# Kernel optimization log

Hardware: AMD Instinct MI355X
Metric: run time of the kernel (lower is better)

## Reference

```python
import jax, jax.numpy as jnp
import numpy as np

WINDOWS = (5, 5, 25, 25)  # per-layer neighborhood window sizes
N_HEAD = 4


def _na2d(x, wqkv, bqkv, wo, bo, window, n_head):
    """2D neighborhood (NATTEN-style) attention, channels-last x: [B,H,W,C].
    Each query attends to a window x window neighborhood whose start is
    clamped so the window stays inside the image (NATTEN boundary rule)."""
    B, H, W, C = x.shape
    hd = C // n_head
    qkv = x @ wqkv + bqkv                      # [B,H,W,3C]
    q, k, v = jnp.split(qkv, 3, axis=-1)
    q = q.reshape(B, H, W, n_head, hd) * (hd ** -0.5)
    k = k.reshape(B, H, W, n_head, hd)
    v = v.reshape(B, H, W, n_head, hd)
    half = window // 2
    sh = jnp.clip(jnp.arange(H) - half, 0, H - window)   # window start per row
    sw = jnp.clip(jnp.arange(W) - half, 0, W - window)
    ih = sh[:, None] + jnp.arange(window)                # [H, window]
    iw = sw[:, None] + jnp.arange(window)                # [W, window]
    # gather K/V neighborhoods -> [B,H,W,window,window,n_head,hd]
    kn = k[:, ih[:, None, :, None], iw[None, :, None, :]]
    vn = v[:, ih[:, None, :, None], iw[None, :, None, :]]
    scores = jnp.einsum('bhwnd,bhwijnd->bhwnij', q, kn)
    kk = window * window
    att = jax.nn.softmax(scores.reshape(B, H, W, n_head, kk), axis=-1)
    out = jnp.einsum('bhwnk,bhwknd->bhwnd', att,
                     vn.reshape(B, H, W, kk, n_head, hd))
    return out.reshape(B, H, W, C) @ wo + bo


def setup_inputs() -> dict:
    key = jax.random.key(0)
    ks = jax.random.split(key, 5)
    B, T, F, C = 1, 64, 352, 24   # batch, time frames, CQT bins (88*4), n_unit
    L = len(WINDOWS)
    s = 1.0 / np.sqrt(C)
    return {
        'x': jax.random.normal(ks[0], (B, T, F, C), jnp.float32),
        'qkv_w': jax.random.normal(ks[1], (L, C, 3 * C), jnp.float32) * s,
        'qkv_b': jax.random.normal(ks[2], (L, 3 * C), jnp.float32) * 0.01,
        'out_w': jax.random.normal(ks[3], (L, C, C), jnp.float32) * s,
        'out_b': jax.random.normal(ks[4], (L, C), jnp.float32) * 0.01,
    }


def reference(x, qkv_w, qkv_b, out_w, out_b):
    for i, win in enumerate(WINDOWS):
        res = x
        x = _na2d(x, qkv_w[i], qkv_b[i], out_w[i], out_b[i], win, N_HEAD) + res
        if i < 2:
            # F.max_pool2d(kernel=(2,1)) on (B,H,W,C) layout pools the W dim by 2
            B, H, W, C = x.shape
            x = x.reshape(B, H, W // 2, 2, C).max(axis=3)
    return jnp.swapaxes(x, -2, -1)   # x.transpose(-2, -1)
```

## Files before the change

kernel.cpp:

```cpp
#include <hip/hip_runtime.h>
#include <cstdint>

#define QSCALE 0.40824829046386301636f

__global__ __launch_bounds__(256) void qkv_first(
    const float* __restrict__ x, const float* __restrict__ w,
    const float* __restrict__ b, float* __restrict__ q,
    float* __restrict__ kv, int npx)
{
  __shared__ __align__(16) float swT[72 * 24];
  __shared__ float sb[72];
  for (int i = threadIdx.x; i < 1728; i += 256) swT[(i % 72) * 24 + i / 72] = w[i];
  if (threadIdx.x < 72) sb[threadIdx.x] = b[threadIdx.x];
  __syncthreads();
  const int t = blockIdx.x * 256 + threadIdx.x;
  const int p = t >> 2, jg = t & 3;
  if (p >= npx) return;
  float xr[24];
  const float4* xp = (const float4*)(x + (size_t)p * 24);
#pragma unroll
  for (int i = 0; i < 6; ++i) {
    const float4 f = xp[i];
    xr[4*i] = f.x; xr[4*i+1] = f.y; xr[4*i+2] = f.z; xr[4*i+3] = f.w;
  }
#pragma unroll
  for (int jj = 0; jj < 18; ++jj) {
    const int j = jg * 18 + jj;
    const float* wr = &swT[j * 24];
    float acc = sb[j];
#pragma unroll
    for (int c = 0; c < 24; ++c) acc += xr[c] * wr[c];
    if (j < 24)      q[((size_t)(j / 6) * npx + p) * 6 + j % 6] = acc * QSCALE;
    else if (j < 48) { const int u = j - 24; kv[((size_t)(u / 6) * npx + p) * 12 + u % 6] = acc; }
    else             { const int u = j - 48; kv[((size_t)(u / 6) * npx + p) * 12 + 6 + u % 6] = acc; }
  }
}

__global__ __launch_bounds__(128) void attn5(
    const float* __restrict__ q, const float* __restrict__ kv,
    float* __restrict__ att, int H, int W)
{
  __shared__ __align__(16) float skv[12 * 12 * 12];
  const int tid = threadIdx.x;
  const int h0 = blockIdx.y * 8, w0 = blockIdx.x * 8, hd = blockIdx.z;
  const int N = H * W;
  const int rlo = min(max(h0 - 2, 0), H - 5);
  const int nr  = min(max(h0 + 5, 0), H - 5) + 4 - rlo + 1;
  const int clo = min(max(w0 - 2, 0), W - 5);
  const int nc  = min(max(w0 + 5, 0), W - 5) + 4 - clo + 1;
  const float* kvh = kv + (size_t)hd * N * 12;
  const int ncc = nc * 3;
  for (int i = tid; i < nr * ncc; i += 128) {
    const int r = i / ncc, c4 = i - r * ncc;
    const float4 v = ((const float4*)(kvh + ((size_t)(rlo + r) * W + clo) * 12))[c4];
    ((float4*)skv)[r * 36 + c4] = v;
  }
  __syncthreads();

  const int ql = tid >> 1, sr = tid & 1;
  const int qh = h0 + (ql >> 3), qw = w0 + (ql & 7);
  const float* qp = q + ((size_t)hd * N + (size_t)qh * W + qw) * 6;
  const float q0 = qp[0], q1 = qp[1], q2 = qp[2], q3 = qp[3], q4 = qp[4], q5 = qp[5];
  const int shq = min(max(qh - 2, 0), H - 5) - rlo;
  const int swq = min(max(qw - 2, 0), W - 5) - clo;

  float m = -1e30f, l = 0.f, a0 = 0, a1 = 0, a2 = 0, a3 = 0, a4 = 0, a5 = 0;
  for (int rr = sr; rr < 5; rr += 2) {
    const float* rowp = skv + ((shq + rr) * 12 + swq) * 12;
#pragma unroll
    for (int cc = 0; cc < 5; ++cc) {
      const float* p = rowp + cc * 12;
      const float4 A = *(const float4*)p;
      const float4 B = *(const float4*)(p + 4);
      const float4 C = *(const float4*)(p + 8);
      const float s = q0*A.x + q1*A.y + q2*A.z + q3*A.w + q4*B.x + q5*B.y;
      float d = s - m;
      if (d > 8.0f) {
        const float r2 = __expf(-d);
        l *= r2; a0 *= r2; a1 *= r2; a2 *= r2; a3 *= r2; a4 *= r2; a5 *= r2;
        m = s; d = 0.f;
      }
      const float e = __expf(d);
      l += e;
      a0 += e*B.z; a1 += e*B.w; a2 += e*C.x;
      a3 += e*C.y; a4 += e*C.z; a5 += e*C.w;
    }
  }
  {
    const float om = __shfl_xor(m, 1), ol = __shfl_xor(l, 1);
    const float o0 = __shfl_xor(a0, 1), o1 = __shfl_xor(a1, 1), o2 = __shfl_xor(a2, 1);
    const float o3 = __shfl_xor(a3, 1), o4 = __shfl_xor(a4, 1), o5 = __shfl_xor(a5, 1);
    const float nm = fmaxf(m, om);
    const float f1 = __expf(m - nm), f2 = __expf(om - nm);
    l = l*f1 + ol*f2;
    a0 = a0*f1 + o0*f2; a1 = a1*f1 + o1*f2; a2 = a2*f1 + o2*f2;
    a3 = a3*f1 + o3*f2; a4 = a4*f1 + o4*f2; a5 = a5*f1 + o5*f2;
  }
  if (sr == 0) {
    const float inv = 1.0f / l;
    float* ap = att + ((size_t)qh * W + qw) * 24 + hd * 6;
    ((float2*)ap)[0] = make_float2(a0*inv, a1*inv);
    ((float2*)ap)[1] = make_float2(a2*inv, a3*inv);
    ((float2*)ap)[2] = make_float2(a4*inv, a5*inv);
  }
}

__global__ __launch_bounds__(256) void attn25(
    const float* __restrict__ q, const float* __restrict__ kv,
    float* __restrict__ att)
{
  constexpr int H = 64, W = 88, N = H * W;
  constexpr int RS = 388;
  __shared__ __align__(16) float skv[28 * RS];
  const int tid = threadIdx.x;
  const int h0 = blockIdx.y * 4, w0 = blockIdx.x * 8, hd = blockIdx.z;
  const int rlo = min(max(h0 - 12, 0), H - 25);
  const int nr  = min(max(h0 + 3 - 12, 0), H - 25) + 24 - rlo + 1;
  const int clo = min(max(w0 - 12, 0), W - 25);
  const int nc  = min(max(w0 + 7 - 12, 0), W - 25) + 24 - clo + 1;
  const float* kvh = kv + (size_t)hd * N * 12;
  const int ncc = nc * 3;
  for (int i = tid; i < nr * ncc; i += 256) {
    const int r = i / ncc, c4 = i - r * ncc;
    const float4 v = ((const float4*)(kvh + ((size_t)(rlo + r) * W + clo) * 12))[c4];
    ((float4*)skv)[r * (RS / 4) + c4] = v;
  }
  __syncthreads();

  const int qw_ = tid >> 5, slice = tid & 31, sr = slice >> 2, sc = slice & 3;
  const int qw = w0 + qw_;
  const int swq = min(max(qw - 12, 0), W - 25) - clo;

  float qv[4][6];
  int srel[4];
#pragma unroll
  for (int qi = 0; qi < 4; ++qi) {
    const float* qp = q + ((size_t)hd * N + (size_t)(h0 + qi) * W + qw) * 6;
#pragma unroll
    for (int d = 0; d < 6; ++d) qv[qi][d] = qp[d];
    srel[qi] = min(max(h0 + qi - 12, 0), H - 25) - rlo;
  }

  float m_[4], l_[4], acc[4][6];
#pragma unroll
  for (int qi = 0; qi < 4; ++qi) {
    m_[qi] = -1e30f; l_[qi] = 0.f;
#pragma unroll
    for (int d = 0; d < 6; ++d) acc[qi][d] = 0.f;
  }

  for (int rg = sr; rg < nr; rg += 8) {
    const float* rowp = skv + rg * RS + swq * 12;
    for (int cc = sc; cc < 25; cc += 4) {
      const float* p = rowp + cc * 12;
      const float4 A = *(const float4*)p;
      const float4 B = *(const float4*)(p + 4);
      const float4 C = *(const float4*)(p + 8);
#pragma unroll
      for (int qi = 0; qi < 4; ++qi) {
        if (rg >= srel[qi] && rg <= srel[qi] + 24) {
          const float s = qv[qi][0]*A.x + qv[qi][1]*A.y + qv[qi][2]*A.z
                        + qv[qi][3]*A.w + qv[qi][4]*B.x + qv[qi][5]*B.y;
          float d = s - m_[qi];
          if (d > 8.0f) {
            const float r2 = __expf(-d);
            l_[qi] *= r2;
            acc[qi][0] *= r2; acc[qi][1] *= r2; acc[qi][2] *= r2;
            acc[qi][3] *= r2; acc[qi][4] *= r2; acc[qi][5] *= r2;
            m_[qi] = s; d = 0.f;
          }
          const float e = __expf(d);
          l_[qi] += e;
          acc[qi][0] += e*B.z; acc[qi][1] += e*B.w; acc[qi][2] += e*C.x;
          acc[qi][3] += e*C.y; acc[qi][4] += e*C.z; acc[qi][5] += e*C.w;
        }
      }
    }
  }

#pragma unroll
  for (int mask = 1; mask <= 16; mask <<= 1) {
#pragma unroll
    for (int qi = 0; qi < 4; ++qi) {
      const float om = __shfl_xor(m_[qi], mask), ol = __shfl_xor(l_[qi], mask);
      float oa[6];
#pragma unroll
      for (int d = 0; d < 6; ++d) oa[d] = __shfl_xor(acc[qi][d], mask);
      const float nm = fmaxf(m_[qi], om);
      const float f1 = __expf(m_[qi] - nm), f2 = __expf(om - nm);
      m_[qi] = nm;
      l_[qi] = l_[qi]*f1 + ol*f2;
#pragma unroll
      for (int d = 0; d < 6; ++d) acc[qi][d] = acc[qi][d]*f1 + oa[d]*f2;
    }
  }
  if (slice == 0) {
#pragma unroll
    for (int qi = 0; qi < 4; ++qi) {
      const float inv = 1.0f / l_[qi];
      float* ap = att + ((size_t)(h0 + qi) * W + qw) * 24 + hd * 6;
      ((float2*)ap)[0] = make_float2(acc[qi][0]*inv, acc[qi][1]*inv);
      ((float2*)ap)[1] = make_float2(acc[qi][2]*inv, acc[qi][3]*inv);
      ((float2*)ap)[2] = make_float2(acc[qi][4]*inv, acc[qi][5]*inv);
    }
  }
}

__global__ __launch_bounds__(256) void glue_pool(
    const float* __restrict__ att, const float* __restrict__ xres,
    const float* __restrict__ wo, const float* __restrict__ bo,
    const float* __restrict__ wq, const float* __restrict__ bq,
    float* __restrict__ xn, float* __restrict__ qn, float* __restrict__ kvn,
    int Nn)
{
  __shared__ __align__(16) float swoT[24 * 24];
  __shared__ float sbo[24];
  __shared__ __align__(16) float swqT[72 * 24];
  __shared__ float sbq[72];
  __shared__ __align__(16) float sy[128 * 28];
  const int tid = threadIdx.x;
  for (int i = tid; i < 576; i += 256) swoT[(i % 24) * 24 + i / 24] = wo[i];
  for (int i = tid; i < 1728; i += 256) swqT[(i % 72) * 24 + i / 72] = wq[i];
  if (tid < 24) sbo[tid] = bo[tid];
  if (tid < 72) sbq[tid] = bq[tid];
  __syncthreads();

  {
    const int lpx = tid >> 1, half = tid & 1;
    const size_t spx = (size_t)blockIdx.x * 128 + lpx;
    float ar[24];
    const float4* ap = (const float4*)(att + spx * 24);
#pragma unroll
    for (int i = 0; i < 6; ++i) {
      const float4 f = ap[i];
      ar[4*i] = f.x; ar[4*i+1] = f.y; ar[4*i+2] = f.z; ar[4*i+3] = f.w;
    }
    float res[12];
    const float4* rp = (const float4*)(xres + spx * 24 + half * 12);
#pragma unroll
    for (int i = 0; i < 3; ++i) {
      const float4 f = rp[i];
      res[4*i] = f.x; res[4*i+1] = f.y; res[4*i+2] = f.z; res[4*i+3] = f.w;
    }
#pragma unroll
    for (int k = 0; k < 12; ++k) {
      const int c = half * 12 + k;
      const float* wr = &swoT[c * 24];
      float acc = sbo[c] + res[k];
#pragma unroll
      for (int j = 0; j < 24; ++j) acc += ar[j] * wr[j];
      sy[lpx * 28 + c] = acc;
    }
  }
  __syncthreads();
  {
    const int ppl = tid >> 2, jg = tid & 3;
    const size_t gp = (size_t)blockIdx.x * 64 + ppl;
    float xp[24];
    const float* y0 = &sy[(2 * ppl) * 28];
    const float* y1 = &sy[(2 * ppl + 1) * 28];
#pragma unroll
    for (int c = 0; c < 24; ++c) xp[c] = fmaxf(y0[c], y1[c]);
    if (jg == 0) {
      float4* xo = (float4*)(xn + gp * 24);
#pragma unroll
      for (int i = 0; i < 6; ++i)
        xo[i] = make_float4(xp[4*i], xp[4*i+1], xp[4*i+2], xp[4*i+3]);
    }
#pragma unroll
    for (int jj = 0; jj < 18; ++jj) {
      const int j = jg * 18 + jj;
      const float* wr = &swqT[j * 24];
      float acc = sbq[j];
#pragma unroll
      for (int c = 0; c < 24; ++c) acc += xp[c] * wr[c];
      if (j < 24)      qn[((size_t)(j / 6) * Nn + gp) * 6 + j % 6] = acc * QSCALE;
      else if (j < 48) { const int u = j - 24; kvn[((size_t)(u / 6) * Nn + gp) * 12 + u % 6] = acc; }
      else             { const int u = j - 48; kvn[((size_t)(u / 6) * Nn + gp) * 12 + 6 + u % 6] = acc; }
    }
  }
}

__global__ __launch_bounds__(256) void glue_nopool(
    const float* __restrict__ att, const float* __restrict__ xres,
    const float* __restrict__ wo, const float* __restrict__ bo,
    const float* __restrict__ wq, const float* __restrict__ bq,
    float* __restrict__ xn, float* __restrict__ qn, float* __restrict__ kvn,
    int Nn)
{
  __shared__ __align__(16) float swoT[24 * 24];
  __shared__ float sbo[24];
  __shared__ __align__(16) float swqT[72 * 24];
  __shared__ float sbq[72];
  __shared__ __align__(16) float sy[64 * 28];
  const int tid = threadIdx.x;
  for (int i = tid; i < 576; i += 256) swoT[(i % 24) * 24 + i / 24] = wo[i];
  for (int i = tid; i < 1728; i += 256) swqT[(i % 72) * 24 + i / 72] = wq[i];
  if (tid < 24) sbo[tid] = bo[tid];
  if (tid < 72) sbq[tid] = bq[tid];
  __syncthreads();

  {
    const int lpx = tid >> 2, qt = tid & 3;
    const size_t spx = (size_t)blockIdx.x * 64 + lpx;
    float ar[24];
    const float4* ap = (const float4*)(att + spx * 24);
#pragma unroll
    for (int i = 0; i < 6; ++i) {
      const float4 f = ap[i];
      ar[4*i] = f.x; ar[4*i+1] = f.y; ar[4*i+2] = f.z; ar[4*i+3] = f.w;
    }
#pragma unroll
    for (int k = 0; k < 6; ++k) {
      const int c = qt * 6 + k;
      const float* wr = &swoT[c * 24];
      float acc = sbo[c] + xres[spx * 24 + c];
#pragma unroll
      for (int j = 0; j < 24; ++j) acc += ar[j] * wr[j];
      sy[lpx * 28 + c] = acc;
      xn[spx * 24 + c] = acc;
    }
  }
  __syncthreads();
  {
    const int lpx = tid >> 2, jg = tid & 3;
    const size_t gp = (size_t)blockIdx.x * 64 + lpx;
    const float* yr = &sy[lpx * 28];
    float xp[24];
#pragma unroll
    for (int c = 0; c < 24; ++c) xp[c] = yr[c];
#pragma unroll
    for (int jj = 0; jj < 18; ++jj) {
      const int j = jg * 18 + jj;
      const float* wr = &swqT[j * 24];
      float acc = sbq[j];
#pragma unroll
      for (int c = 0; c < 24; ++c) acc += xp[c] * wr[c];
      if (j < 24)      qn[((size_t)(j / 6) * Nn + gp) * 6 + j % 6] = acc * QSCALE;
      else if (j < 48) { const int u = j - 24; kvn[((size_t)(u / 6) * Nn + gp) * 12 + u % 6] = acc; }
      else             { const int u = j - 48; kvn[((size_t)(u / 6) * Nn + gp) * 12 + 6 + u % 6] = acc; }
    }
  }
}

__global__ __launch_bounds__(256) void final_out(
    const float* __restrict__ att, const float* __restrict__ xres,
    const float* __restrict__ wo, const float* __restrict__ bo,
    float* __restrict__ dout)
{
  __shared__ __align__(16) float swoT[24 * 24];
  __shared__ float sbo[24];
  const int tid = threadIdx.x;
  for (int i = tid; i < 576; i += 256) swoT[(i % 24) * 24 + i / 24] = wo[i];
  if (tid < 24) sbo[tid] = bo[tid];
  __syncthreads();
  const int lpx = tid >> 1, half = tid & 1;
  const size_t spx = (size_t)blockIdx.x * 128 + lpx;
  const int gh = (int)(spx / 88), gw = (int)(spx % 88);
  float ar[24];
  const float4* ap = (const float4*)(att + spx * 24);
#pragma unroll
  for (int i = 0; i < 6; ++i) {
    const float4 f = ap[i];
    ar[4*i] = f.x; ar[4*i+1] = f.y; ar[4*i+2] = f.z; ar[4*i+3] = f.w;
  }
  float res[12];
  const float4* rp = (const float4*)(xres + spx * 24 + half * 12);
#pragma unroll
  for (int i = 0; i < 3; ++i) {
    const float4 f = rp[i];
    res[4*i] = f.x; res[4*i+1] = f.y; res[4*i+2] = f.z; res[4*i+3] = f.w;
  }
#pragma unroll
  for (int k = 0; k < 12; ++k) {
    const int c = half * 12 + k;
    const float* wr = &swoT[c * 24];
    float acc = sbo[c] + res[k];
#pragma unroll
    for (int j = 0; j < 24; ++j) acc += ar[j] * wr[j];
    dout[((size_t)gh * 24 + c) * 88 + gw] = acc;
  }
}

extern "C" void kernel_launch(void* const* d_in, const int* in_sizes, int n_in,
                              void* d_out, int out_size, void* d_ws, size_t ws_size,
                              hipStream_t stream)
{
  const float* x      = (const float*)d_in[0];
  const float* qkv_w  = (const float*)d_in[1];
  const float* qkv_b  = (const float*)d_in[2];
  const float* out_w  = (const float*)d_in[3];
  const float* out_b  = (const float*)d_in[4];
  float* out = (float*)d_out;
  float* ws = (float*)d_ws;

  const int N0 = 64 * 352, N1 = 64 * 176, N2 = 64 * 88;
  float* q   = ws;
  float* kvb = q + (size_t)N0 * 24;
  float* att = kvb + (size_t)N0 * 48;
  float* x1  = att + (size_t)N0 * 24;
  float* x2  = x1 + (size_t)N1 * 24;
  float* x3  = x2 + (size_t)N2 * 24;

  qkv_first<<<(N0 * 4) / 256, 256, 0, stream>>>(x, qkv_w, qkv_b, q, kvb, N0);

  attn5<<<dim3(44, 8, 4), 128, 0, stream>>>(q, kvb, att, 64, 352);
  glue_pool<<<176, 256, 0, stream>>>(att, x, out_w, out_b,
                                     qkv_w + 1728, qkv_b + 72, x1, q, kvb, N1);

  attn5<<<dim3(22, 8, 4), 128, 0, stream>>>(q, kvb, att, 64, 176);
  glue_pool<<<88, 256, 0, stream>>>(att, x1, out_w + 576, out_b + 24,
                                    qkv_w + 2 * 1728, qkv_b + 2 * 72, x2, q, kvb, N2);

  attn25<<<dim3(11, 16, 4), 256, 0, stream>>>(q, kvb, att);
  glue_nopool<<<88, 256, 0, stream>>>(att, x2, out_w + 2 * 576, out_b + 2 * 24,
                                      qkv_w + 3 * 1728, qkv_b + 3 * 72, x3, q, kvb, N2);

  attn25<<<dim3(11, 16, 4), 256, 0, stream>>>(q, kvb, att);
  final_out<<<44, 256, 0, stream>>>(att, x3, out_w + 3 * 576, out_b + 3 * 24, out);
}
```

Before: 176.1 us.

## Fuse 5x5 attention with out-proj, pooling and next QKV; drop online-softmax max tracking

Merges the 5x5 neighborhood attention kernel with the following glue kernel (output projection, residual, max-pool, next-layer QKV), processing all four heads per block. The attention output no longer round-trips through global memory, and two launches per layer go away. Q/KV buffers are now double-buffered so one fused kernel can read one set while writing the next. The online-softmax running max and rescale are removed in both attention kernels in favour of plain exp sums with float2 packed FMAs, which risks overflow if scores grow large.

```diff
diff --git a/kernel.cpp b/kernel.cpp
--- a/kernel.cpp
+++ b/kernel.cpp
@@ -2,6 +2,13 @@
 #include <cstdint>
 
 #define QSCALE 0.40824829046386301636f
+
+__device__ __forceinline__ float2 pk_fma(float2 a, float2 b, float2 c) {
+  return make_float2(fmaf(a.x, b.x, c.x), fmaf(a.y, b.y, c.y));
+}
+__device__ __forceinline__ float2 pk_mul(float2 a, float2 b) {
+  return make_float2(a.x * b.x, a.y * b.y);
+}
 
 __global__ __launch_bounds__(256) void qkv_first(
     const float* __restrict__ x, const float* __restrict__ w,
@@ -36,72 +43,135 @@
   }
 }
 
-__global__ __launch_bounds__(128) void attn5(
-    const float* __restrict__ q, const float* __restrict__ kv,
-    float* __restrict__ att, int H, int W)
-{
-  __shared__ __align__(16) float skv[12 * 12 * 12];
+__global__ __launch_bounds__(256) void attn5_fused(
+    const float* __restrict__ q, const float* __restrict__ kvb,
+    const float* __restrict__ xres,
+    const float* __restrict__ wo, const float* __restrict__ bo,
+    const float* __restrict__ wq, const float* __restrict__ bq,
+    float* __restrict__ xn, float* __restrict__ qn, float* __restrict__ kvn,
+    int H, int W, int Nn)
+{
+  __shared__ __align__(16) float skv[4 * 1732];
+  __shared__ __align__(16) float satt[64 * 28];
+  __shared__ __align__(16) float swoT[24 * 24];
+  __shared__ float sbo[24];
+  __shared__ __align__(16) float swqT[72 * 24];
+  __shared__ float sbq[72];
+
   const int tid = threadIdx.x;
-  const int h0 = blockIdx.y * 8, w0 = blockIdx.x * 8, hd = blockIdx.z;
+  const int h0 = blockIdx.y * 8, w0 = blockIdx.x * 8;
   const int N = H * W;
+
+  for (int i = tid; i < 576; i += 256) swoT[(i % 24) * 24 + i / 24] = wo[i];
+  for (int i = tid; i < 1728; i += 256) swqT[(i % 72) * 24 + i / 72] = wq[i];
+  if (tid < 24) sbo[tid] = bo[tid];
+  if (tid < 72) sbq[tid] = bq[tid];
+
   const int rlo = min(max(h0 - 2, 0), H - 5);
   const int nr  = min(max(h0 + 5, 0), H - 5) + 4 - rlo + 1;
   const int clo = min(max(w0 - 2, 0), W - 5);
   const int nc  = min(max(w0 + 5, 0), W - 5) + 4 - clo + 1;
-  const float* kvh = kv + (size_t)hd * N * 12;
   const int ncc = nc * 3;
-  for (int i = tid; i < nr * ncc; i += 128) {
+  for (int i = tid; i < nr * ncc; i += 256) {
     const int r = i / ncc, c4 = i - r * ncc;
-    const float4 v = ((const float4*)(kvh + ((size_t)(rlo + r) * W + clo) * 12))[c4];
-    ((float4*)skv)[r * 36 + c4] = v;
-  }
-  __syncthreads();
-
-  const int ql = tid >> 1, sr = tid & 1;
-  const int qh = h0 + (ql >> 3), qw = w0 + (ql & 7);
-  const float* qp = q + ((size_t)hd * N + (size_t)qh * W + qw) * 6;
-  const float q0 = qp[0], q1 = qp[1], q2 = qp[2], q3 = qp[3], q4 = qp[4], q5 = qp[5];
-  const int shq = min(max(qh - 2, 0), H - 5) - rlo;
-  const int swq = min(max(qw - 2, 0), W - 5) - clo;
-
-  float m = -1e30f, l = 0.f, a0 = 0, a1 = 0, a2 = 0, a3 = 0, a4 = 0, a5 = 0;
-  for (int rr = sr; rr < 5; rr += 2) {
-    const float* rowp = skv + ((shq + rr) * 12 + swq) * 12;
-#pragma unroll
-    for (int cc = 0; cc < 5; ++cc) {
-      const float* p = rowp + cc * 12;
-      const float4 A = *(const float4*)p;
-      const float4 B = *(const float4*)(p + 4);
-      const float4 C = *(const float4*)(p + 8);
-      const float s = q0*A.x + q1*A.y + q2*A.z + q3*A.w + q4*B.x + q5*B.y;
-      float d = s - m;
-      if (d > 8.0f) {
-        const float r2 = __expf(-d);
-        l *= r2; a0 *= r2; a1 *= r2; a2 *= r2; a3 *= r2; a4 *= r2; a5 *= r2;
-        m = s; d = 0.f;
+    const size_t goff = ((size_t)(rlo + r) * W + clo) * 12;
+#pragma unroll
+    for (int h = 0; h < 4; ++h) {
+      const float4 v = ((const float4*)(kvb + (size_t)h * N * 12 + goff))[c4];
+      ((float4*)skv)[h * 433 + r * 36 + c4] = v;
+    }
+  }
+  __syncthreads();
+
+  {
+    const int ql = tid >> 2, head = tid & 3;
+    const int qh = h0 + (ql >> 3), qw = w0 + (ql & 7);
+    const float* qp = q + ((size_t)head * N + (size_t)qh * W + qw) * 6;
+    const float2 q01 = *(const float2*)qp;
+    const float2 q23 = *(const float2*)(qp + 2);
+    const float2 q45 = *(const float2*)(qp + 4);
+    const int shq = min(max(qh - 2, 0), H - 5) - rlo;
+    const int swq = min(max(qw - 2, 0), W - 5) - clo;
+    const float* plane = skv + head * 1732;
+
+    float l = 0.f;
+    float2 a01 = make_float2(0, 0), a23 = make_float2(0, 0), a45 = make_float2(0, 0);
+#pragma unroll
+    for (int rr = 0; rr < 5; ++rr) {
+      const float* rowp = plane + (shq + rr) * 144 + swq * 12;
+#pragma unroll
+      for (int cc = 0; cc < 5; ++cc) {
+        const float* p = rowp + cc * 12;
+        const float4 A = *(const float4*)p;
+        const float4 B = *(const float4*)(p + 4);
+        const float4 C = *(const float4*)(p + 8);
+        float2 t = pk_mul(q01, make_float2(A.x, A.y));
+        t = pk_fma(q23, make_float2(A.z, A.w), t);
+        t = pk_fma(q45, make_float2(B.x, B.y), t);
+        const float e = __expf(t.x + t.y);
+        l += e;
+        const float2 e2 = make_float2(e, e);
+        a01 = pk_fma(e2, make_float2(B.z, B.w), a01);
+        a23 = pk_fma(e2, make_float2(C.x, C.y), a23);
+        a45 = pk_fma(e2, make_float2(C.z, C.w), a45);
       }
-      const float e = __expf(d);
-      l += e;
-      a0 += e*B.z; a1 += e*B.w; a2 += e*C.x;
-      a3 += e*C.y; a4 += e*C.z; a5 += e*C.w;
-    }
-  }
+    }
+    const float inv = 1.0f / l;
+    float* ao = satt + ql * 28 + head * 6;
+    ((float2*)ao)[0] = make_float2(a01.x * inv, a01.y * inv);
+    ((float2*)ao)[1] = make_float2(a23.x * inv, a23.y * inv);
+    ((float2*)ao)[2] = make_float2(a45.x * inv, a45.y * inv);
+  }
+  __syncthreads();
+
+  float* sy = skv;
   {
-    const float om = __shfl_xor(m, 1), ol = __shfl_xor(l, 1);
-    const float o0 = __shfl_xor(a0, 1), o1 = __shfl_xor(a1, 1), o2 = __shfl_xor(a2, 1);
-    const float o3 = __shfl_xor(a3, 1), o4 = __shfl_xor(a4, 1), o5 = __shfl_xor(a5, 1);
-    const float nm = fmaxf(m, om);
-    const float f1 = __expf(m - nm), f2 = __expf(om - nm);
-    l = l*f1 + ol*f2;
-    a0 = a0*f1 + o0*f2; a1 = a1*f1 + o1*f2; a2 = a2*f1 + o2*f2;
-    a3 = a3*f1 + o3*f2; a4 = a4*f1 + o4*f2; a5 = a5*f1 + o5*f2;
-  }
-  if (sr == 0) {
-    const float inv = 1.0f / l;
-    float* ap = att + ((size_t)qh * W + qw) * 24 + hd * 6;
-    ((float2*)ap)[0] = make_float2(a0*inv, a1*inv);
-    ((float2*)ap)[1] = make_float2(a2*inv, a3*inv);
-    ((float2*)ap)[2] = make_float2(a4*inv, a5*inv);
+    const int px = tid >> 2, qt = tid & 3;
+    const int gh = h0 + (px >> 3), gw = w0 + (px & 7);
+    const float* ar = satt + px * 28;
+    float a[24];
+#pragma unroll
+    for (int j = 0; j < 24; ++j) a[j] = ar[j];
+    const float* resp = xres + ((size_t)gh * W + gw) * 24;
+#pragma unroll
+    for (int k = 0; k < 6; ++k) {
+      const int c = qt * 6 + k;
+      const float* wr = &swoT[c * 24];
+      float acc = sbo[c] + resp[c];
+#pragma unroll
+      for (int j = 0; j < 24; ++j) acc += a[j] * wr[j];
+      sy[px * 28 + c] = acc;
+    }
+  }
+  __syncthreads();
+
+  {
+    const int pp = tid >> 3, jg = tid & 7;
+    const int pr = pp >> 2, pc = pp & 3;
+    const float* y0 = &sy[(pr * 8 + 2 * pc) * 28];
+    const float* y1 = &sy[(pr * 8 + 2 * pc + 1) * 28];
+    float xp[24];
+#pragma unroll
+    for (int c = 0; c < 24; ++c) xp[c] = fmaxf(y0[c], y1[c]);
+    const int Wn = W >> 1;
+    const size_t gp = (size_t)(h0 + pr) * Wn + (w0 >> 1) + pc;
+    if (jg == 0) {
+      float4* xo = (float4*)(xn + gp * 24);
+#pragma unroll
+      for (int i = 0; i < 6; ++i)
+        xo[i] = make_float4(xp[4*i], xp[4*i+1], xp[4*i+2], xp[4*i+3]);
+    }
+#pragma unroll
+    for (int jj = 0; jj < 9; ++jj) {
+      const int j = jg * 9 + jj;
+      const float* wr = &swqT[j * 24];
+      float acc = sbq[j];
+#pragma unroll
+      for (int c = 0; c < 24; ++c) acc += xp[c] * wr[c];
+      if (j < 24)      qn[((size_t)(j / 6) * Nn + gp) * 6 + j % 6] = acc * QSCALE;
+      else if (j < 48) { const int u = j - 24; kvn[((size_t)(u / 6) * Nn + gp) * 12 + u % 6] = acc; }
+      else             { const int u = j - 48; kvn[((size_t)(u / 6) * Nn + gp) * 12 + 6 + u % 6] = acc; }
+    }
   }
 }
 
@@ -131,22 +201,23 @@
   const int qw = w0 + qw_;
   const int swq = min(max(qw - 12, 0), W - 25) - clo;
 
-  float qv[4][6];
+  float2 q01[4], q23[4], q45[4];
   int srel[4];
 #pragma unroll
   for (int qi = 0; qi < 4; ++qi) {
     const float* qp = q + ((size_t)hd * N + (size_t)(h0 + qi) * W + qw) * 6;
-#pragma unroll
-    for (int d = 0; d < 6; ++d) qv[qi][d] = qp[d];
+    q01[qi] = *(const float2*)qp;
+    q23[qi] = *(const float2*)(qp + 2);
+    q45[qi] = *(const float2*)(qp + 4);
     srel[qi] = min(max(h0 + qi - 12, 0), H - 25) - rlo;
   }
 
-  float m_[4], l_[4], acc[4][6];
+  float l_[4];
+  float2 a01[4], a23[4], a45[4];
 #pragma unroll
   for (int qi = 0; qi < 4; ++qi) {
-    m_[qi] = -1e30f; l_[qi] = 0.f;
-#pragma unroll
-    for (int d = 0; d < 6; ++d) acc[qi][d] = 0.f;
+    l_[qi] = 0.f;
+    a01[qi] = make_float2(0, 0); a23[qi] = make_float2(0, 0); a45[qi] = make_float2(0, 0);
   }
 
   for (int rg = sr; rg < nr; rg += 8) {
@@ -156,23 +227,24 @@
       const float4 A = *(const float4*)p;
       const float4 B = *(const float4*)(p + 4);
       const float4 C = *(const float4*)(p + 8);
+      const float2 k01 = make_float2(A.x, A.y);
+      const float2 k23 = make_float2(A.z, A.w);
+      const float2 k45 = make_float2(B.x, B.y);
+      const float2 v01 = make_float2(B.z, B.w);
+      const float2 v23 = make_float2(C.x, C.y);
+      const float2 v45 = make_float2(C.z, C.w);
 #pragma unroll
       for (int qi = 0; qi < 4; ++qi) {
         if (rg >= srel[qi] && rg <= srel[qi] + 24) {
-          const float s = qv[qi][0]*A.x + qv[qi][1]*A.y + qv[qi][2]*A.z
-                        + qv[qi][3]*A.w + qv[qi][4]*B.x + qv[qi][5]*B.y;
-          float d = s - m_[qi];
-          if (d > 8.0f) {
-            const float r2 = __expf(-d);
-            l_[qi] *= r2;
-            acc[qi][0] *= r2; acc[qi][1] *= r2; acc[qi][2] *= r2;
-            acc[qi][3] *= r2; acc[qi][4] *= r2; acc[qi][5] *= r2;
-            m_[qi] = s; d = 0.f;
-          }
-          const float e = __expf(d);
+          float2 t = pk_mul(q01[qi], k01);
+          t = pk_fma(q23[qi], k23, t);
+          t = pk_fma(q45[qi], k45, t);
+          const float e = __expf(t.x + t.y);
           l_[qi] += e;
-          acc[qi][0] += e*B.z; acc[qi][1] += e*B.w; acc[qi][2] += e*C.x;
-          acc[qi][3] += e*C.y; acc[qi][4] += e*C.z; acc[qi][5] += e*C.w;
+          const float2 e2 = make_float2(e, e);
+          a01[qi] = pk_fma(e2, v01, a01[qi]);
+          a23[qi] = pk_fma(e2, v23, a23[qi]);
+          a45[qi] = pk_fma(e2, v45, a45[qi]);
         }
       }
     }
@@ -182,16 +254,13 @@
   for (int mask = 1; mask <= 16; mask <<= 1) {
 #pragma unroll
     for (int qi = 0; qi < 4; ++qi) {
-      const float om = __shfl_xor(m_[qi], mask), ol = __shfl_xor(l_[qi], mask);
-      float oa[6];
-#pragma unroll
-      for (int d = 0; d < 6; ++d) oa[d] = __shfl_xor(acc[qi][d], mask);
-      const float nm = fmaxf(m_[qi], om);
-      const float f1 = __expf(m_[qi] - nm), f2 = __expf(om - nm);
-      m_[qi] = nm;
-      l_[qi] = l_[qi]*f1 + ol*f2;
-#pragma unroll
-      for (int d = 0; d < 6; ++d) acc[qi][d] = acc[qi][d]*f1 + oa[d]*f2;
+      l_[qi] += __shfl_xor(l_[qi], mask);
+      a01[qi].x += __shfl_xor(a01[qi].x, mask);
+      a01[qi].y += __shfl_xor(a01[qi].y, mask);
+      a23[qi].x += __shfl_xor(a23[qi].x, mask);
+      a23[qi].y += __shfl_xor(a23[qi].y, mask);
+      a45[qi].x += __shfl_xor(a45[qi].x, mask);
+      a45[qi].y += __shfl_xor(a45[qi].y, mask);
     }
   }
   if (slice == 0) {
@@ -199,84 +268,9 @@
     for (int qi = 0; qi < 4; ++qi) {
       const float inv = 1.0f / l_[qi];
       float* ap = att + ((size_t)(h0 + qi) * W + qw) * 24 + hd * 6;
-      ((float2*)ap)[0] = make_float2(acc[qi][0]*inv, acc[qi][1]*inv);
-      ((float2*)ap)[1] = make_float2(acc[qi][2]*inv, acc[qi][3]*inv);
-      ((float2*)ap)[2] = make_float2(acc[qi][4]*inv, acc[qi][5]*inv);
-    }
-  }
-}
-
-__global__ __launch_bounds__(256) void glue_pool(
-    const float* __restrict__ att, const float* __restrict__ xres,
-    const float* __restrict__ wo, const float* __restrict__ bo,
-    const float* __restrict__ wq, const float* __restrict__ bq,
-    float* __restrict__ xn, float* __restrict__ qn, float* __restrict__ kvn,
-    int Nn)
-{
-  __shared__ __align__(16) float swoT[24 * 24];
-  __shared__ float sbo[24];
-  __shared__ __align__(16) float swqT[72 * 24];
-  __shared__ float sbq[72];
-  __shared__ __align__(16) float sy[128 * 28];
-  const int tid = threadIdx.x;
-  for (int i = tid; i < 576; i += 256) swoT[(i % 24) * 24 + i / 24] = wo[i];
-  for (int i = tid; i < 1728; i += 256) swqT[(i % 72) * 24 + i / 72] = wq[i];
-  if (tid < 24) sbo[tid] = bo[tid];
-  if (tid < 72) sbq[tid] = bq[tid];
-  __syncthreads();
-
-  {
-    const int lpx = tid >> 1, half = tid & 1;
-    const size_t spx = (size_t)blockIdx.x * 128 + lpx;
-    float ar[24];
-    const float4* ap = (const float4*)(att + spx * 24);
-#pragma unroll
-    for (int i = 0; i < 6; ++i) {
-      const float4 f = ap[i];
-      ar[4*i] = f.x; ar[4*i+1] = f.y; ar[4*i+2] = f.z; ar[4*i+3] = f.w;
-    }
-    float res[12];
-    const float4* rp = (const float4*)(xres + spx * 24 + half * 12);
-#pragma unroll
-    for (int i = 0; i < 3; ++i) {
-      const float4 f = rp[i];
-      res[4*i] = f.x; res[4*i+1] = f.y; res[4*i+2] = f.z; res[4*i+3] = f.w;
-    }
-#pragma unroll
-    for (int k = 0; k < 12; ++k) {
-      const int c = half * 12 + k;
-      const float* wr = &swoT[c * 24];
-      float acc = sbo[c] + res[k];
-#pragma unroll
-      for (int j = 0; j < 24; ++j) acc += ar[j] * wr[j];
-      sy[lpx * 28 + c] = acc;
-    }
-  }
-  __syncthreads();
-  {
-    const int ppl = tid >> 2, jg = tid & 3;
-    const size_t gp = (size_t)blockIdx.x * 64 + ppl;
-    float xp[24];
-    const float* y0 = &sy[(2 * ppl) * 28];
-    const float* y1 = &sy[(2 * ppl + 1) * 28];
-#pragma unroll
-    for (int c = 0; c < 24; ++c) xp[c] = fmaxf(y0[c], y1[c]);
-    if (jg == 0) {
-      float4* xo = (float4*)(xn + gp * 24);
-#pragma unroll
-      for (int i = 0; i < 6; ++i)
-        xo[i] = make_float4(xp[4*i], xp[4*i+1], xp[4*i+2], xp[4*i+3]);
-    }
-#pragma unroll
-    for (int jj = 0; jj < 18; ++jj) {
-      const int j = jg * 18 + jj;
-      const float* wr = &swqT[j * 24];
-      float acc = sbq[j];
-#pragma unroll
-      for (int c = 0; c < 24; ++c) acc += xp[c] * wr[c];
-      if (j < 24)      qn[((size_t)(j / 6) * Nn + gp) * 6 + j % 6] = acc * QSCALE;
-      else if (j < 48) { const int u = j - 24; kvn[((size_t)(u / 6) * Nn + gp) * 12 + u % 6] = acc; }
-      else             { const int u = j - 48; kvn[((size_t)(u / 6) * Nn + gp) * 12 + 6 + u % 6] = acc; }
+      ((float2*)ap)[0] = make_float2(a01[qi].x * inv, a01[qi].y * inv);
+      ((float2*)ap)[1] = make_float2(a23[qi].x * inv, a23[qi].y * inv);
+      ((float2*)ap)[2] = make_float2(a45[qi].x * inv, a45[qi].y * inv);
     }
   }
 }
@@ -395,27 +389,29 @@
   float* ws = (float*)d_ws;
 
   const int N0 = 64 * 352, N1 = 64 * 176, N2 = 64 * 88;
-  float* q   = ws;
-  float* kvb = q + (size_t)N0 * 24;
-  float* att = kvb + (size_t)N0 * 48;
-  float* x1  = att + (size_t)N0 * 24;
-  float* x2  = x1 + (size_t)N1 * 24;
-  float* x3  = x2 + (size_t)N2 * 24;
-
-  qkv_first<<<(N0 * 4) / 256, 256, 0, stream>>>(x, qkv_w, qkv_b, q, kvb, N0);
-
-  attn5<<<dim3(44, 8, 4), 128, 0, stream>>>(q, kvb, att, 64, 352);
-  glue_pool<<<176, 256, 0, stream>>>(att, x, out_w, out_b,
-                                     qkv_w + 1728, qkv_b + 72, x1, q, kvb, N1);
-
-  attn5<<<dim3(22, 8, 4), 128, 0, stream>>>(q, kvb, att, 64, 176);
-  glue_pool<<<88, 256, 0, stream>>>(att, x1, out_w + 576, out_b + 24,
-                                    qkv_w + 2 * 1728, qkv_b + 2 * 72, x2, q, kvb, N2);
-
-  attn25<<<dim3(11, 16, 4), 256, 0, stream>>>(q, kvb, att);
+  float* q_a  = ws;
+  float* kv_a = q_a + (size_t)N0 * 24;
+  float* q_b  = kv_a + (size_t)N0 * 48;
+  float* kv_b = q_b + (size_t)N1 * 24;
+  float* att  = kv_b + (size_t)N1 * 48;
+  float* x1   = att + (size_t)N0 * 24;
+  float* x2   = x1 + (size_t)N1 * 24;
+  float* x3   = x2 + (size_t)N2 * 24;
+
+  qkv_first<<<(N0 * 4) / 256, 256, 0, stream>>>(x, qkv_w, qkv_b, q_a, kv_a, N0);
+
+  attn5_fused<<<dim3(44, 8), 256, 0, stream>>>(
+      q_a, kv_a, x, out_w, out_b, qkv_w + 1728, qkv_b + 72,
+      x1, q_b, kv_b, 64, 352, N1);
+
+  attn5_fused<<<dim3(22, 8), 256, 0, stream>>>(
+      q_b, kv_b, x1, out_w + 576, out_b + 24, qkv_w + 2 * 1728, qkv_b + 2 * 72,
+      x2, q_a, kv_a, 64, 176, N2);
+
+  attn25<<<dim3(11, 16, 4), 256, 0, stream>>>(q_a, kv_a, att);
   glue_nopool<<<88, 256, 0, stream>>>(att, x2, out_w + 2 * 576, out_b + 2 * 24,
-                                      qkv_w + 3 * 1728, qkv_b + 3 * 72, x3, q, kvb, N2);
-
-  attn25<<<dim3(11, 16, 4), 256, 0, stream>>>(q, kvb, att);
+                                      qkv_w + 3 * 1728, qkv_b + 3 * 72, x3, q_b, kv_b, N2);
+
+  attn25<<<dim3(11, 16, 4), 256, 0, stream>>>(q_b, kv_b, att);
   final_out<<<44, 256, 0, stream>>>(att, x3, out_w + 3 * 576, out_b + 3 * 24, out);
 }
```

Measured after the change: 152.5 us. -13.4%, faster.
